# Performance work log

Hardware: AMD Instinct MI355X
Metric: run time of the kernel (lower is better)

## Reference

```python
import jax, jax.numpy as jnp
import numpy as np

N_EXPERTS = 8
D_MODEL = 1024
D_FF = 4096


def setup_inputs() -> dict:
    key = jax.random.key(0)
    k_x, k_idx, k_g, k_u, k_d = jax.random.split(key, 5)
    scale_in = 1.0 / np.sqrt(D_MODEL)
    scale_ff = 1.0 / np.sqrt(D_FF)
    return {
        "x": jax.random.normal(k_x, (2, 1024, D_MODEL), dtype=jnp.float32),
        "expert_idx": jax.random.randint(k_idx, (2, 1024), 0, N_EXPERTS, dtype=jnp.int64),
        "w_gate": jax.random.normal(k_g, (N_EXPERTS, D_MODEL, D_FF), dtype=jnp.float32) * scale_in,
        "w_up": jax.random.normal(k_u, (N_EXPERTS, D_MODEL, D_FF), dtype=jnp.float32) * scale_in,
        "w_down": jax.random.normal(k_d, (N_EXPERTS, D_FF, D_MODEL), dtype=jnp.float32) * scale_ff,
    }


def reference(x, expert_idx, w_gate, w_up, w_down):
    # x: [B, S, D]; expert_idx: [B, S] in [0, N_EXPERTS)
    B, S, D = x.shape
    x_flat = x.reshape(-1, D)                  # [T, D]
    idx_flat = expert_idx.reshape(-1)          # [T]
    out = jnp.zeros_like(x_flat)
    # Faithful per-expert dispatch: each token is processed by exactly one
    # expert's SwiGLU FFN; masked scatter-back combines results.
    for e in range(N_EXPERTS):
        mask = (idx_flat == e)[:, None]        # [T, 1]
        gate = jax.nn.silu(x_flat @ w_gate[e]) # [T, F]
        up = x_flat @ w_up[e]                  # [T, F]
        y = (gate * up) @ w_down[e]            # [T, D]
        out = jnp.where(mask, y, out)
    return out.reshape(B, S, D)
```

## Files before the change

kernel.cpp:

```cpp
#include <hip/hip_runtime.h>
#include <hip/hip_bf16.h>
#include <stdint.h>

#define N_EXPERTS 8
#define D_MODEL   1024
#define D_FF      4096
#define T_TOKENS  2048
#define MT1       128
#define MAXT1     24
#define MT2       64
#define MAXT2     40
#define BK        64
#define KP        72

typedef __attribute__((ext_vector_type(8))) short bf16x8;
typedef __attribute__((ext_vector_type(4))) float f32x4;

__device__ __forceinline__ short f2bf(float f) {
    union { float f; uint32_t u; } v; v.f = f;
    uint32_t u = v.u;
    return (short)((u + 0x7fffu + ((u >> 16) & 1u)) >> 16);
}

__device__ __forceinline__ uint32_t pack2bf(float a, float b) {
    __hip_bfloat162 h = __float22bfloat162_rn(make_float2(a, b));
    return *(uint32_t*)&h;
}

template<int STRIDE>
__device__ __forceinline__ void ldw16(float v[16], const float* __restrict__ src) {
#pragma unroll
    for (int j = 0; j < 16; ++j) v[j] = src[(size_t)j * STRIDE];
}

__device__ __forceinline__ void stw16(short* dst, const float v[16]) {
    uint4 w0, w1;
    w0.x = pack2bf(v[0], v[1]);  w0.y = pack2bf(v[2], v[3]);
    w0.z = pack2bf(v[4], v[5]);  w0.w = pack2bf(v[6], v[7]);
    w1.x = pack2bf(v[8], v[9]);  w1.y = pack2bf(v[10], v[11]);
    w1.z = pack2bf(v[12], v[13]); w1.w = pack2bf(v[14], v[15]);
    *(uint4*)dst = w0;
    *(uint4*)(dst + 8) = w1;
}


__global__ void moe_route(const int* __restrict__ idx, int* __restrict__ offsets,
                          int* __restrict__ nt1p, int* __restrict__ t1_e,
                          int* __restrict__ t1_p0, int* __restrict__ t1_end,
                          int* __restrict__ nt2p, int* __restrict__ t2_e,
                          int* __restrict__ t2_p0, int* __restrict__ t2_end) {
    __shared__ int cnt[N_EXPERTS];
    int tid = threadIdx.x;
    if (tid < N_EXPERTS) cnt[tid] = 0;
    __syncthreads();
    for (int t = tid; t < T_TOKENS; t += 256) atomicAdd(&cnt[idx[t]], 1);
    __syncthreads();
    if (tid == 0) {
        int off = 0, nt1 = 0, nt2 = 0;
        for (int e = 0; e < N_EXPERTS; ++e) {
            offsets[e] = off;
            int c = cnt[e], end = off + c;
            for (int i = 0; i < c; i += MT1) { t1_e[nt1] = e; t1_p0[nt1] = off + i; t1_end[nt1] = end; ++nt1; }
            for (int i = 0; i < c; i += MT2) { t2_e[nt2] = e; t2_p0[nt2] = off + i; t2_end[nt2] = end; ++nt2; }
            off = end;
        }
        offsets[N_EXPERTS] = off;
        *nt1p = nt1;
        *nt2p = nt2;
    }
}

__global__ void moe_gather(const float* __restrict__ x, const int* __restrict__ idx,
                           const int* __restrict__ offsets, int* __restrict__ cursor,
                           int* __restrict__ tok_of_row, short* __restrict__ Xg) {
    __shared__ int sp;
    int t = blockIdx.x;
    if (threadIdx.x == 0) {
        int e = idx[t];
        int p = offsets[e] + atomicAdd(&cursor[e], 1);
        tok_of_row[p] = t;
        sp = p;
    }
    __syncthreads();
    int p = sp;
    const float4* src = (const float4*)(x + (size_t)t * D_MODEL);
    uint2* dst = (uint2*)(Xg + (size_t)p * D_MODEL);
    int i = threadIdx.x;
    float4 v = src[i];
    uint2 o;
    o.x = pack2bf(v.x, v.y);
    o.y = pack2bf(v.z, v.w);
    dst[i] = o;
}


__launch_bounds__(256)
__global__ void moe_gemm1(const float* __restrict__ wg, const float* __restrict__ wu,
                          const short* __restrict__ Xg, short* __restrict__ h,
                          const int* __restrict__ tile_e, const int* __restrict__ tile_p0,
                          const int* __restrict__ tile_end, const int* __restrict__ ntiles) {
    int ti = blockIdx.y;
    if (ti >= *ntiles) return;
    int e = tile_e[ti], p0 = tile_p0[ti], pend = tile_end[ti];
    int n0 = blockIdx.x * 64;

    __shared__ short Bg[2][64][KP];
    __shared__ short Bu[2][64][KP];

    int tid = threadIdx.x;
    int nl = tid & 63, kc = tid >> 6;
    int lane = tid & 63, w = tid >> 6;
    int col = lane & 15, quad = lane >> 4;

    const float* wgb = wg + (size_t)e * D_MODEL * D_FF + (size_t)(kc * 16) * D_FF + n0 + nl;
    const float* wub = wu + (size_t)e * D_MODEL * D_FF + (size_t)(kc * 16) * D_FF + n0 + nl;

    int row0 = p0 + w * 32 + col;      if (row0 > T_TOKENS - 1) row0 = T_TOKENS - 1;
    int row1 = row0 + 16;              if (row1 > T_TOKENS - 1) row1 = T_TOKENS - 1;
    const short* a0p = Xg + (size_t)row0 * D_MODEL + quad * 8;
    const short* a1p = Xg + (size_t)row1 * D_MODEL + quad * 8;

    f32x4 accg[2][4], accu[2][4];
#pragma unroll
    for (int m = 0; m < 2; ++m)
#pragma unroll
        for (int nf = 0; nf < 4; ++nf) {
            accg[m][nf] = (f32x4){0,0,0,0};
            accu[m][nf] = (f32x4){0,0,0,0};
        }

    {
        float g0[16], u0[16];
        ldw16<D_FF>(g0, wgb);
        ldw16<D_FF>(u0, wub);
        stw16(&Bg[0][nl][kc * 16], g0);
        stw16(&Bu[0][nl][kc * 16], u0);
    }
    __syncthreads();

    bf16x8 a00 = *(const bf16x8*)(a0p);
    bf16x8 a01 = *(const bf16x8*)(a0p + 32);
    bf16x8 a10 = *(const bf16x8*)(a1p);
    bf16x8 a11 = *(const bf16x8*)(a1p + 32);

    const int NIT = D_MODEL / BK;
    int p = 0;
#pragma unroll 1
    for (int it = 0; it < NIT; ++it) {
        int kn = (it + 1 == NIT) ? 0 : (it + 1) * BK;
        float gn[16], un[16];
        ldw16<D_FF>(gn, wgb + (size_t)kn * D_FF);
        ldw16<D_FF>(un, wub + (size_t)kn * D_FF);
        bf16x8 a00n = *(const bf16x8*)(a0p + kn);
        bf16x8 a01n = *(const bf16x8*)(a0p + kn + 32);
        bf16x8 a10n = *(const bf16x8*)(a1p + kn);
        bf16x8 a11n = *(const bf16x8*)(a1p + kn + 32);

#pragma unroll
        for (int nf = 0; nf < 4; ++nf) {
            bf16x8 bg0 = *(const bf16x8*)&Bg[p][nf * 16 + col][quad * 8];
            bf16x8 bg1 = *(const bf16x8*)&Bg[p][nf * 16 + col][32 + quad * 8];
            bf16x8 bu0 = *(const bf16x8*)&Bu[p][nf * 16 + col][quad * 8];
            bf16x8 bu1 = *(const bf16x8*)&Bu[p][nf * 16 + col][32 + quad * 8];
            accg[0][nf] = __builtin_amdgcn_mfma_f32_16x16x32_bf16(a00, bg0, accg[0][nf], 0, 0, 0);
            accg[0][nf] = __builtin_amdgcn_mfma_f32_16x16x32_bf16(a01, bg1, accg[0][nf], 0, 0, 0);
            accg[1][nf] = __builtin_amdgcn_mfma_f32_16x16x32_bf16(a10, bg0, accg[1][nf], 0, 0, 0);
            accg[1][nf] = __builtin_amdgcn_mfma_f32_16x16x32_bf16(a11, bg1, accg[1][nf], 0, 0, 0);
            accu[0][nf] = __builtin_amdgcn_mfma_f32_16x16x32_bf16(a00, bu0, accu[0][nf], 0, 0, 0);
            accu[0][nf] = __builtin_amdgcn_mfma_f32_16x16x32_bf16(a01, bu1, accu[0][nf], 0, 0, 0);
            accu[1][nf] = __builtin_amdgcn_mfma_f32_16x16x32_bf16(a10, bu0, accu[1][nf], 0, 0, 0);
            accu[1][nf] = __builtin_amdgcn_mfma_f32_16x16x32_bf16(a11, bu1, accu[1][nf], 0, 0, 0);
        }

        stw16(&Bg[p ^ 1][nl][kc * 16], gn);
        stw16(&Bu[p ^ 1][nl][kc * 16], un);
        a00 = a00n; a01 = a01n; a10 = a10n; a11 = a11n;
        __syncthreads();
        p ^= 1;
    }

#pragma unroll
    for (int m = 0; m < 2; ++m) {
#pragma unroll
        for (int r = 0; r < 4; ++r) {
            int mr = p0 + w * 32 + m * 16 + quad * 4 + r;
            if (mr < pend) {
#pragma unroll
                for (int nf = 0; nf < 4; ++nf) {
                    float gv = accg[m][nf][r], uv = accu[m][nf][r];
                    float hv = (gv / (1.f + __expf(-gv))) * uv;
                    h[(size_t)mr * D_FF + n0 + nf * 16 + col] = f2bf(hv);
                }
            }
        }
    }
}


__launch_bounds__(256)
__global__ void moe_gemm2(const float* __restrict__ wd, const short* __restrict__ h,
                          const int* __restrict__ tok_of_row, float* __restrict__ out,
                          const int* __restrict__ tile_e, const int* __restrict__ tile_p0,
                          const int* __restrict__ tile_end, const int* __restrict__ ntiles) {
    int ti = blockIdx.y;
    if (ti >= *ntiles) return;
    int e = tile_e[ti], p0 = tile_p0[ti], pend = tile_end[ti];
    int d0 = blockIdx.x * 64;

    __shared__ short Bd[2][64][KP];

    int tid = threadIdx.x;
    int nl = tid & 63, kc = tid >> 6;
    int lane = tid & 63, w = tid >> 6;
    int col = lane & 15, quad = lane >> 4;

    const float* wb = wd + (size_t)e * D_FF * D_MODEL + (size_t)(kc * 16) * D_MODEL + d0 + nl;

    int row0 = p0 + w * 16 + col;      if (row0 > T_TOKENS - 1) row0 = T_TOKENS - 1;
    const short* a0p = h + (size_t)row0 * D_FF + quad * 8;

    f32x4 acc[4];
#pragma unroll
    for (int nf = 0; nf < 4; ++nf) acc[nf] = (f32x4){0,0,0,0};

    {
        float w0[16];
        ldw16<D_MODEL>(w0, wb);
        stw16(&Bd[0][nl][kc * 16], w0);
    }
    __syncthreads();

    bf16x8 a0 = *(const bf16x8*)(a0p);
    bf16x8 a1 = *(const bf16x8*)(a0p + 32);

    const int NIT = D_FF / BK;
    int p = 0;
#pragma unroll 1
    for (int it = 0; it < NIT; ++it) {
        int kn = (it + 1 == NIT) ? 0 : (it + 1) * BK;
        float wn[16];
        ldw16<D_MODEL>(wn, wb + (size_t)kn * D_MODEL);
        bf16x8 a0n = *(const bf16x8*)(a0p + kn);
        bf16x8 a1n = *(const bf16x8*)(a0p + kn + 32);

#pragma unroll
        for (int nf = 0; nf < 4; ++nf) {
            bf16x8 b0 = *(const bf16x8*)&Bd[p][nf * 16 + col][quad * 8];
            bf16x8 b1 = *(const bf16x8*)&Bd[p][nf * 16 + col][32 + quad * 8];
            acc[nf] = __builtin_amdgcn_mfma_f32_16x16x32_bf16(a0, b0, acc[nf], 0, 0, 0);
            acc[nf] = __builtin_amdgcn_mfma_f32_16x16x32_bf16(a1, b1, acc[nf], 0, 0, 0);
        }

        stw16(&Bd[p ^ 1][nl][kc * 16], wn);
        a0 = a0n; a1 = a1n;
        __syncthreads();
        p ^= 1;
    }

#pragma unroll
    for (int r = 0; r < 4; ++r) {
        int mr = p0 + w * 16 + quad * 4 + r;
        if (mr < pend) {
            int t = tok_of_row[mr];
#pragma unroll
            for (int nf = 0; nf < 4; ++nf)
                out[(size_t)t * D_MODEL + d0 + nf * 16 + col] = acc[nf][r];
        }
    }
}


extern "C" void kernel_launch(void* const* d_in, const int* in_sizes, int n_in,
                              void* d_out, int out_size, void* d_ws, size_t ws_size,
                              hipStream_t stream) {
    (void)in_sizes; (void)n_in; (void)out_size; (void)ws_size;
    const float* x   = (const float*)d_in[0];
    const int*   idx = (const int*)d_in[1];
    const float* wg  = (const float*)d_in[2];
    const float* wu  = (const float*)d_in[3];
    const float* wd  = (const float*)d_in[4];
    float* out = (float*)d_out;

    int* ws_i       = (int*)d_ws;
    int* cursor     = ws_i;
    int* offsets    = ws_i + 8;
    int* nt1        = ws_i + 20;
    int* nt2        = ws_i + 21;
    int* t1_e       = ws_i + 32;
    int* t1_p0      = ws_i + 56;
    int* t1_end     = ws_i + 80;
    int* t2_e       = ws_i + 104;
    int* t2_p0      = ws_i + 144;
    int* t2_end     = ws_i + 184;
    int* tok_of_row = ws_i + 256;

    short* Xg = (short*)((char*)d_ws + 16384);
    short* h  = (short*)((char*)d_ws + 16384 + (size_t)T_TOKENS * D_MODEL * 2);

    hipMemsetAsync(d_ws, 0, 128, stream);
    moe_route<<<dim3(1), 256, 0, stream>>>(idx, offsets, nt1, t1_e, t1_p0, t1_end,
                                           nt2, t2_e, t2_p0, t2_end);
    moe_gather<<<dim3(T_TOKENS), 256, 0, stream>>>(x, idx, offsets, cursor, tok_of_row, Xg);
    moe_gemm1<<<dim3(D_FF / 64, MAXT1), 256, 0, stream>>>(wg, wu, Xg, h,
                                                          t1_e, t1_p0, t1_end, nt1);
    moe_gemm2<<<dim3(D_MODEL / 64, MAXT2), 256, 0, stream>>>(wd, h, tok_of_row, out,
                                                             t2_e, t2_p0, t2_end, nt2);
}
```

Before: 508.0 us.

## Enlarge token tiles to 256 rows and split-K the down projection with atomics

Both GEMMs now use 256-token tiles, with each wave covering 64 rows, so every fp32 weight tile loaded and converted into LDS is reused across more tokens. This cuts repeated weight reads, which dominate traffic, especially in the down projection that previously used 64-row tiles. To keep enough blocks in flight, the down projection splits K into 8 slices that accumulate into a zero-initialised output via float atomicAdd. The trade-offs are higher register pressure, an extra memset, atomic contention, and slightly nondeterministic summation order.

```diff
diff --git a/kernel.cpp b/kernel.cpp
--- a/kernel.cpp
+++ b/kernel.cpp
@@ -6,10 +6,9 @@
 #define D_MODEL   1024
 #define D_FF      4096
 #define T_TOKENS  2048
-#define MT1       128
-#define MAXT1     24
-#define MT2       64
-#define MAXT2     40
+#define MT        256
+#define MAXT      16
+#define KSPLIT    8
 #define BK        64
 #define KP        72
 
@@ -45,10 +44,8 @@
 
 
 __global__ void moe_route(const int* __restrict__ idx, int* __restrict__ offsets,
-                          int* __restrict__ nt1p, int* __restrict__ t1_e,
-                          int* __restrict__ t1_p0, int* __restrict__ t1_end,
-                          int* __restrict__ nt2p, int* __restrict__ t2_e,
-                          int* __restrict__ t2_p0, int* __restrict__ t2_end) {
+                          int* __restrict__ ntp, int* __restrict__ t_e,
+                          int* __restrict__ t_p0, int* __restrict__ t_end) {
     __shared__ int cnt[N_EXPERTS];
     int tid = threadIdx.x;
     if (tid < N_EXPERTS) cnt[tid] = 0;
@@ -56,17 +53,15 @@
     for (int t = tid; t < T_TOKENS; t += 256) atomicAdd(&cnt[idx[t]], 1);
     __syncthreads();
     if (tid == 0) {
-        int off = 0, nt1 = 0, nt2 = 0;
+        int off = 0, nt = 0;
         for (int e = 0; e < N_EXPERTS; ++e) {
             offsets[e] = off;
             int c = cnt[e], end = off + c;
-            for (int i = 0; i < c; i += MT1) { t1_e[nt1] = e; t1_p0[nt1] = off + i; t1_end[nt1] = end; ++nt1; }
-            for (int i = 0; i < c; i += MT2) { t2_e[nt2] = e; t2_p0[nt2] = off + i; t2_end[nt2] = end; ++nt2; }
+            for (int i = 0; i < c; i += MT) { t_e[nt] = e; t_p0[nt] = off + i; t_end[nt] = end; ++nt; }
             off = end;
         }
         offsets[N_EXPERTS] = off;
-        *nt1p = nt1;
-        *nt2p = nt2;
+        *ntp = nt;
     }
 }
 
@@ -94,14 +89,14 @@
 }
 
 
-__launch_bounds__(256)
+__launch_bounds__(256, 2)
 __global__ void moe_gemm1(const float* __restrict__ wg, const float* __restrict__ wu,
                           const short* __restrict__ Xg, short* __restrict__ h,
-                          const int* __restrict__ tile_e, const int* __restrict__ tile_p0,
-                          const int* __restrict__ tile_end, const int* __restrict__ ntiles) {
+                          const int* __restrict__ t_e, const int* __restrict__ t_p0,
+                          const int* __restrict__ t_end, const int* __restrict__ ntp) {
     int ti = blockIdx.y;
-    if (ti >= *ntiles) return;
-    int e = tile_e[ti], p0 = tile_p0[ti], pend = tile_end[ti];
+    if (ti >= *ntp) return;
+    int e = t_e[ti], p0 = t_p0[ti], pend = t_end[ti];
     int n0 = blockIdx.x * 64;
 
     __shared__ short Bg[2][64][KP];
@@ -115,14 +110,17 @@
     const float* wgb = wg + (size_t)e * D_MODEL * D_FF + (size_t)(kc * 16) * D_FF + n0 + nl;
     const float* wub = wu + (size_t)e * D_MODEL * D_FF + (size_t)(kc * 16) * D_FF + n0 + nl;
 
-    int row0 = p0 + w * 32 + col;      if (row0 > T_TOKENS - 1) row0 = T_TOKENS - 1;
-    int row1 = row0 + 16;              if (row1 > T_TOKENS - 1) row1 = T_TOKENS - 1;
-    const short* a0p = Xg + (size_t)row0 * D_MODEL + quad * 8;
-    const short* a1p = Xg + (size_t)row1 * D_MODEL + quad * 8;
-
-    f32x4 accg[2][4], accu[2][4];
-#pragma unroll
-    for (int m = 0; m < 2; ++m)
+    const short* ap[4];
+#pragma unroll
+    for (int m = 0; m < 4; ++m) {
+        int r = p0 + w * 64 + m * 16 + col;
+        if (r > T_TOKENS - 1) r = T_TOKENS - 1;
+        ap[m] = Xg + (size_t)r * D_MODEL + quad * 8;
+    }
+
+    f32x4 accg[4][4], accu[4][4];
+#pragma unroll
+    for (int m = 0; m < 4; ++m)
 #pragma unroll
         for (int nf = 0; nf < 4; ++nf) {
             accg[m][nf] = (f32x4){0,0,0,0};
@@ -137,11 +135,6 @@
         stw16(&Bu[0][nl][kc * 16], u0);
     }
     __syncthreads();
-
-    bf16x8 a00 = *(const bf16x8*)(a0p);
-    bf16x8 a01 = *(const bf16x8*)(a0p + 32);
-    bf16x8 a10 = *(const bf16x8*)(a1p);
-    bf16x8 a11 = *(const bf16x8*)(a1p + 32);
 
     const int NIT = D_MODEL / BK;
     int p = 0;
@@ -151,39 +144,40 @@
         float gn[16], un[16];
         ldw16<D_FF>(gn, wgb + (size_t)kn * D_FF);
         ldw16<D_FF>(un, wub + (size_t)kn * D_FF);
-        bf16x8 a00n = *(const bf16x8*)(a0p + kn);
-        bf16x8 a01n = *(const bf16x8*)(a0p + kn + 32);
-        bf16x8 a10n = *(const bf16x8*)(a1p + kn);
-        bf16x8 a11n = *(const bf16x8*)(a1p + kn + 32);
-
-#pragma unroll
-        for (int nf = 0; nf < 4; ++nf) {
-            bf16x8 bg0 = *(const bf16x8*)&Bg[p][nf * 16 + col][quad * 8];
-            bf16x8 bg1 = *(const bf16x8*)&Bg[p][nf * 16 + col][32 + quad * 8];
-            bf16x8 bu0 = *(const bf16x8*)&Bu[p][nf * 16 + col][quad * 8];
-            bf16x8 bu1 = *(const bf16x8*)&Bu[p][nf * 16 + col][32 + quad * 8];
-            accg[0][nf] = __builtin_amdgcn_mfma_f32_16x16x32_bf16(a00, bg0, accg[0][nf], 0, 0, 0);
-            accg[0][nf] = __builtin_amdgcn_mfma_f32_16x16x32_bf16(a01, bg1, accg[0][nf], 0, 0, 0);
-            accg[1][nf] = __builtin_amdgcn_mfma_f32_16x16x32_bf16(a10, bg0, accg[1][nf], 0, 0, 0);
-            accg[1][nf] = __builtin_amdgcn_mfma_f32_16x16x32_bf16(a11, bg1, accg[1][nf], 0, 0, 0);
-            accu[0][nf] = __builtin_amdgcn_mfma_f32_16x16x32_bf16(a00, bu0, accu[0][nf], 0, 0, 0);
-            accu[0][nf] = __builtin_amdgcn_mfma_f32_16x16x32_bf16(a01, bu1, accu[0][nf], 0, 0, 0);
-            accu[1][nf] = __builtin_amdgcn_mfma_f32_16x16x32_bf16(a10, bu0, accu[1][nf], 0, 0, 0);
-            accu[1][nf] = __builtin_amdgcn_mfma_f32_16x16x32_bf16(a11, bu1, accu[1][nf], 0, 0, 0);
+        int kb = it * BK;
+
+#pragma unroll
+        for (int ks = 0; ks < 2; ++ks) {
+            bf16x8 a0 = *(const bf16x8*)(ap[0] + kb + ks * 32);
+            bf16x8 a1 = *(const bf16x8*)(ap[1] + kb + ks * 32);
+            bf16x8 a2 = *(const bf16x8*)(ap[2] + kb + ks * 32);
+            bf16x8 a3 = *(const bf16x8*)(ap[3] + kb + ks * 32);
+#pragma unroll
+            for (int nf = 0; nf < 4; ++nf) {
+                bf16x8 bg = *(const bf16x8*)&Bg[p][nf * 16 + col][ks * 32 + quad * 8];
+                bf16x8 bu = *(const bf16x8*)&Bu[p][nf * 16 + col][ks * 32 + quad * 8];
+                accg[0][nf] = __builtin_amdgcn_mfma_f32_16x16x32_bf16(a0, bg, accg[0][nf], 0, 0, 0);
+                accg[1][nf] = __builtin_amdgcn_mfma_f32_16x16x32_bf16(a1, bg, accg[1][nf], 0, 0, 0);
+                accg[2][nf] = __builtin_amdgcn_mfma_f32_16x16x32_bf16(a2, bg, accg[2][nf], 0, 0, 0);
+                accg[3][nf] = __builtin_amdgcn_mfma_f32_16x16x32_bf16(a3, bg, accg[3][nf], 0, 0, 0);
+                accu[0][nf] = __builtin_amdgcn_mfma_f32_16x16x32_bf16(a0, bu, accu[0][nf], 0, 0, 0);
+                accu[1][nf] = __builtin_amdgcn_mfma_f32_16x16x32_bf16(a1, bu, accu[1][nf], 0, 0, 0);
+                accu[2][nf] = __builtin_amdgcn_mfma_f32_16x16x32_bf16(a2, bu, accu[2][nf], 0, 0, 0);
+                accu[3][nf] = __builtin_amdgcn_mfma_f32_16x16x32_bf16(a3, bu, accu[3][nf], 0, 0, 0);
+            }
         }
 
         stw16(&Bg[p ^ 1][nl][kc * 16], gn);
         stw16(&Bu[p ^ 1][nl][kc * 16], un);
-        a00 = a00n; a01 = a01n; a10 = a10n; a11 = a11n;
         __syncthreads();
         p ^= 1;
     }
 
 #pragma unroll
-    for (int m = 0; m < 2; ++m) {
+    for (int m = 0; m < 4; ++m) {
 #pragma unroll
         for (int r = 0; r < 4; ++r) {
-            int mr = p0 + w * 32 + m * 16 + quad * 4 + r;
+            int mr = p0 + w * 64 + m * 16 + quad * 4 + r;
             if (mr < pend) {
 #pragma unroll
                 for (int nf = 0; nf < 4; ++nf) {
@@ -197,15 +191,16 @@
 }
 
 
-__launch_bounds__(256)
+__launch_bounds__(256, 3)
 __global__ void moe_gemm2(const float* __restrict__ wd, const short* __restrict__ h,
                           const int* __restrict__ tok_of_row, float* __restrict__ out,
-                          const int* __restrict__ tile_e, const int* __restrict__ tile_p0,
-                          const int* __restrict__ tile_end, const int* __restrict__ ntiles) {
+                          const int* __restrict__ t_e, const int* __restrict__ t_p0,
+                          const int* __restrict__ t_end, const int* __restrict__ ntp) {
     int ti = blockIdx.y;
-    if (ti >= *ntiles) return;
-    int e = tile_e[ti], p0 = tile_p0[ti], pend = tile_end[ti];
+    if (ti >= *ntp) return;
+    int e = t_e[ti], p0 = t_p0[ti], pend = t_end[ti];
     int d0 = blockIdx.x * 64;
+    int Koff = blockIdx.z * (D_FF / KSPLIT);
 
     __shared__ short Bd[2][64][KP];
 
@@ -214,14 +209,21 @@
     int lane = tid & 63, w = tid >> 6;
     int col = lane & 15, quad = lane >> 4;
 
-    const float* wb = wd + (size_t)e * D_FF * D_MODEL + (size_t)(kc * 16) * D_MODEL + d0 + nl;
-
-    int row0 = p0 + w * 16 + col;      if (row0 > T_TOKENS - 1) row0 = T_TOKENS - 1;
-    const short* a0p = h + (size_t)row0 * D_FF + quad * 8;
-
-    f32x4 acc[4];
-#pragma unroll
-    for (int nf = 0; nf < 4; ++nf) acc[nf] = (f32x4){0,0,0,0};
+    const float* wb = wd + (size_t)e * D_FF * D_MODEL + (size_t)(Koff + kc * 16) * D_MODEL + d0 + nl;
+
+    const short* ap[4];
+#pragma unroll
+    for (int m = 0; m < 4; ++m) {
+        int r = p0 + w * 64 + m * 16 + col;
+        if (r > T_TOKENS - 1) r = T_TOKENS - 1;
+        ap[m] = h + (size_t)r * D_FF + Koff + quad * 8;
+    }
+
+    f32x4 acc[4][4];
+#pragma unroll
+    for (int m = 0; m < 4; ++m)
+#pragma unroll
+        for (int nf = 0; nf < 4; ++nf) acc[m][nf] = (f32x4){0,0,0,0};
 
     {
         float w0[16];
@@ -230,41 +232,47 @@
     }
     __syncthreads();
 
-    bf16x8 a0 = *(const bf16x8*)(a0p);
-    bf16x8 a1 = *(const bf16x8*)(a0p + 32);
-
-    const int NIT = D_FF / BK;
+    const int NIT = (D_FF / KSPLIT) / BK;
     int p = 0;
 #pragma unroll 1
     for (int it = 0; it < NIT; ++it) {
         int kn = (it + 1 == NIT) ? 0 : (it + 1) * BK;
         float wn[16];
         ldw16<D_MODEL>(wn, wb + (size_t)kn * D_MODEL);
-        bf16x8 a0n = *(const bf16x8*)(a0p + kn);
-        bf16x8 a1n = *(const bf16x8*)(a0p + kn + 32);
-
-#pragma unroll
-        for (int nf = 0; nf < 4; ++nf) {
-            bf16x8 b0 = *(const bf16x8*)&Bd[p][nf * 16 + col][quad * 8];
-            bf16x8 b1 = *(const bf16x8*)&Bd[p][nf * 16 + col][32 + quad * 8];
-            acc[nf] = __builtin_amdgcn_mfma_f32_16x16x32_bf16(a0, b0, acc[nf], 0, 0, 0);
-            acc[nf] = __builtin_amdgcn_mfma_f32_16x16x32_bf16(a1, b1, acc[nf], 0, 0, 0);
+        int kb = it * BK;
+
+#pragma unroll
+        for (int ks = 0; ks < 2; ++ks) {
+            bf16x8 a0 = *(const bf16x8*)(ap[0] + kb + ks * 32);
+            bf16x8 a1 = *(const bf16x8*)(ap[1] + kb + ks * 32);
+            bf16x8 a2 = *(const bf16x8*)(ap[2] + kb + ks * 32);
+            bf16x8 a3 = *(const bf16x8*)(ap[3] + kb + ks * 32);
+#pragma unroll
+            for (int nf = 0; nf < 4; ++nf) {
+                bf16x8 b = *(const bf16x8*)&Bd[p][nf * 16 + col][ks * 32 + quad * 8];
+                acc[0][nf] = __builtin_amdgcn_mfma_f32_16x16x32_bf16(a0, b, acc[0][nf], 0, 0, 0);
+                acc[1][nf] = __builtin_amdgcn_mfma_f32_16x16x32_bf16(a1, b, acc[1][nf], 0, 0, 0);
+                acc[2][nf] = __builtin_amdgcn_mfma_f32_16x16x32_bf16(a2, b, acc[2][nf], 0, 0, 0);
+                acc[3][nf] = __builtin_amdgcn_mfma_f32_16x16x32_bf16(a3, b, acc[3][nf], 0, 0, 0);
+            }
         }
 
         stw16(&Bd[p ^ 1][nl][kc * 16], wn);
-        a0 = a0n; a1 = a1n;
         __syncthreads();
         p ^= 1;
     }
 
 #pragma unroll
-    for (int r = 0; r < 4; ++r) {
-        int mr = p0 + w * 16 + quad * 4 + r;
-        if (mr < pend) {
-            int t = tok_of_row[mr];
-#pragma unroll
-            for (int nf = 0; nf < 4; ++nf)
-                out[(size_t)t * D_MODEL + d0 + nf * 16 + col] = acc[nf][r];
+    for (int m = 0; m < 4; ++m) {
+#pragma unroll
+        for (int r = 0; r < 4; ++r) {
+            int mr = p0 + w * 64 + m * 16 + quad * 4 + r;
+            if (mr < pend) {
+                int t = tok_of_row[mr];
+#pragma unroll
+                for (int nf = 0; nf < 4; ++nf)
+                    atomicAdd(&out[(size_t)t * D_MODEL + d0 + nf * 16 + col], acc[m][nf][r]);
+            }
         }
     }
 }
@@ -284,25 +292,21 @@
     int* ws_i       = (int*)d_ws;
     int* cursor     = ws_i;
     int* offsets    = ws_i + 8;
-    int* nt1        = ws_i + 20;
-    int* nt2        = ws_i + 21;
-    int* t1_e       = ws_i + 32;
-    int* t1_p0      = ws_i + 56;
-    int* t1_end     = ws_i + 80;
-    int* t2_e       = ws_i + 104;
-    int* t2_p0      = ws_i + 144;
-    int* t2_end     = ws_i + 184;
+    int* nt         = ws_i + 20;
+    int* t_e        = ws_i + 32;
+    int* t_p0       = ws_i + 48;
+    int* t_end      = ws_i + 64;
     int* tok_of_row = ws_i + 256;
 
     short* Xg = (short*)((char*)d_ws + 16384);
     short* h  = (short*)((char*)d_ws + 16384 + (size_t)T_TOKENS * D_MODEL * 2);
 
     hipMemsetAsync(d_ws, 0, 128, stream);
-    moe_route<<<dim3(1), 256, 0, stream>>>(idx, offsets, nt1, t1_e, t1_p0, t1_end,
-                                           nt2, t2_e, t2_p0, t2_end);
+    hipMemsetAsync(out, 0, (size_t)T_TOKENS * D_MODEL * sizeof(float), stream);
+    moe_route<<<dim3(1), 256, 0, stream>>>(idx, offsets, nt, t_e, t_p0, t_end);
     moe_gather<<<dim3(T_TOKENS), 256, 0, stream>>>(x, idx, offsets, cursor, tok_of_row, Xg);
-    moe_gemm1<<<dim3(D_FF / 64, MAXT1), 256, 0, stream>>>(wg, wu, Xg, h,
-                                                          t1_e, t1_p0, t1_end, nt1);
-    moe_gemm2<<<dim3(D_MODEL / 64, MAXT2), 256, 0, stream>>>(wd, h, tok_of_row, out,
-                                                             t2_e, t2_p0, t2_end, nt2);
-}
+    moe_gemm1<<<dim3(D_FF / 64, MAXT), 256, 0, stream>>>(wg, wu, Xg, h,
+                                                         t_e, t_p0, t_end, nt);
+    moe_gemm2<<<dim3(D_MODEL / 64, MAXT, KSPLIT), 256, 0, stream>>>(wd, h, tok_of_row, out,
+                                                                    t_e, t_p0, t_end, nt);
+}
```

After: 559.6 us. +10.2%, slower.

## Split gemm1 gate/up across 512-thread blocks and split-K gemm2 with atomics

Applied to the files above, without the earlier changes.

gemm1 now launches 512 threads per block, with half the waves computing the gate projection and half the up projection. The SiLU gate values are exchanged through shared memory, which halves per-wave accumulator registers and doubles the waves per block. gemm2 splits the D_FF reduction four ways over a grid z dimension and accumulates into a zeroed output with float atomicAdd. This raises parallelism for the small-N down projection, at the cost of an output memset, atomic traffic and non-deterministic summation order.

```diff
diff --git a/kernel.cpp b/kernel.cpp
--- a/kernel.cpp
+++ b/kernel.cpp
@@ -10,6 +10,7 @@
 #define MAXT1     24
 #define MT2       64
 #define MAXT2     40
+#define KSPLIT    4
 #define BK        64
 #define KP        72
 
@@ -94,7 +95,7 @@
 }
 
 
-__launch_bounds__(256)
+__launch_bounds__(512)
 __global__ void moe_gemm1(const float* __restrict__ wg, const float* __restrict__ wu,
                           const short* __restrict__ Xg, short* __restrict__ h,
                           const int* __restrict__ tile_e, const int* __restrict__ tile_p0,
@@ -104,37 +105,35 @@
     int e = tile_e[ti], p0 = tile_p0[ti], pend = tile_end[ti];
     int n0 = blockIdx.x * 64;
 
-    __shared__ short Bg[2][64][KP];
-    __shared__ short Bu[2][64][KP];
+    __shared__ short Bsh[2][2][64][KP];
 
     int tid = threadIdx.x;
-    int nl = tid & 63, kc = tid >> 6;
+    int st = tid & 255, matS = tid >> 8;
+    int nl = st & 63, kc = st >> 6;
     int lane = tid & 63, w = tid >> 6;
+    int mat = w >> 2, wm = w & 3;
     int col = lane & 15, quad = lane >> 4;
 
-    const float* wgb = wg + (size_t)e * D_MODEL * D_FF + (size_t)(kc * 16) * D_FF + n0 + nl;
-    const float* wub = wu + (size_t)e * D_MODEL * D_FF + (size_t)(kc * 16) * D_FF + n0 + nl;
-
-    int row0 = p0 + w * 32 + col;      if (row0 > T_TOKENS - 1) row0 = T_TOKENS - 1;
+    const float* wsrc = (matS ? wu : wg) + (size_t)e * D_MODEL * D_FF
+                        + (size_t)(kc * 16) * D_FF + n0 + nl;
+    short* std0 = &Bsh[matS][0][nl][kc * 16];
+    short* std1 = &Bsh[matS][1][nl][kc * 16];
+
+    int row0 = p0 + wm * 32 + col;     if (row0 > T_TOKENS - 1) row0 = T_TOKENS - 1;
     int row1 = row0 + 16;              if (row1 > T_TOKENS - 1) row1 = T_TOKENS - 1;
     const short* a0p = Xg + (size_t)row0 * D_MODEL + quad * 8;
     const short* a1p = Xg + (size_t)row1 * D_MODEL + quad * 8;
 
-    f32x4 accg[2][4], accu[2][4];
+    f32x4 acc[2][4];
 #pragma unroll
     for (int m = 0; m < 2; ++m)
 #pragma unroll
-        for (int nf = 0; nf < 4; ++nf) {
-            accg[m][nf] = (f32x4){0,0,0,0};
-            accu[m][nf] = (f32x4){0,0,0,0};
-        }
+        for (int nf = 0; nf < 4; ++nf) acc[m][nf] = (f32x4){0,0,0,0};
 
     {
-        float g0[16], u0[16];
-        ldw16<D_FF>(g0, wgb);
-        ldw16<D_FF>(u0, wub);
-        stw16(&Bg[0][nl][kc * 16], g0);
-        stw16(&Bu[0][nl][kc * 16], u0);
+        float g0[16];
+        ldw16<D_FF>(g0, wsrc);
+        stw16(std0, g0);
     }
     __syncthreads();
 
@@ -142,15 +141,16 @@
     bf16x8 a01 = *(const bf16x8*)(a0p + 32);
     bf16x8 a10 = *(const bf16x8*)(a1p);
     bf16x8 a11 = *(const bf16x8*)(a1p + 32);
+
+    auto Bp = Bsh[mat];
 
     const int NIT = D_MODEL / BK;
     int p = 0;
 #pragma unroll 1
     for (int it = 0; it < NIT; ++it) {
         int kn = (it + 1 == NIT) ? 0 : (it + 1) * BK;
-        float gn[16], un[16];
-        ldw16<D_FF>(gn, wgb + (size_t)kn * D_FF);
-        ldw16<D_FF>(un, wub + (size_t)kn * D_FF);
+        float gn[16];
+        ldw16<D_FF>(gn, wsrc + (size_t)kn * D_FF);
         bf16x8 a00n = *(const bf16x8*)(a0p + kn);
         bf16x8 a01n = *(const bf16x8*)(a0p + kn + 32);
         bf16x8 a10n = *(const bf16x8*)(a1p + kn);
@@ -158,41 +158,50 @@
 
 #pragma unroll
         for (int nf = 0; nf < 4; ++nf) {
-            bf16x8 bg0 = *(const bf16x8*)&Bg[p][nf * 16 + col][quad * 8];
-            bf16x8 bg1 = *(const bf16x8*)&Bg[p][nf * 16 + col][32 + quad * 8];
-            bf16x8 bu0 = *(const bf16x8*)&Bu[p][nf * 16 + col][quad * 8];
-            bf16x8 bu1 = *(const bf16x8*)&Bu[p][nf * 16 + col][32 + quad * 8];
-            accg[0][nf] = __builtin_amdgcn_mfma_f32_16x16x32_bf16(a00, bg0, accg[0][nf], 0, 0, 0);
-            accg[0][nf] = __builtin_amdgcn_mfma_f32_16x16x32_bf16(a01, bg1, accg[0][nf], 0, 0, 0);
-            accg[1][nf] = __builtin_amdgcn_mfma_f32_16x16x32_bf16(a10, bg0, accg[1][nf], 0, 0, 0);
-            accg[1][nf] = __builtin_amdgcn_mfma_f32_16x16x32_bf16(a11, bg1, accg[1][nf], 0, 0, 0);
-            accu[0][nf] = __builtin_amdgcn_mfma_f32_16x16x32_bf16(a00, bu0, accu[0][nf], 0, 0, 0);
-            accu[0][nf] = __builtin_amdgcn_mfma_f32_16x16x32_bf16(a01, bu1, accu[0][nf], 0, 0, 0);
-            accu[1][nf] = __builtin_amdgcn_mfma_f32_16x16x32_bf16(a10, bu0, accu[1][nf], 0, 0, 0);
-            accu[1][nf] = __builtin_amdgcn_mfma_f32_16x16x32_bf16(a11, bu1, accu[1][nf], 0, 0, 0);
+            bf16x8 b0 = *(const bf16x8*)&Bp[p][nf * 16 + col][quad * 8];
+            bf16x8 b1 = *(const bf16x8*)&Bp[p][nf * 16 + col][32 + quad * 8];
+            acc[0][nf] = __builtin_amdgcn_mfma_f32_16x16x32_bf16(a00, b0, acc[0][nf], 0, 0, 0);
+            acc[0][nf] = __builtin_amdgcn_mfma_f32_16x16x32_bf16(a01, b1, acc[0][nf], 0, 0, 0);
+            acc[1][nf] = __builtin_amdgcn_mfma_f32_16x16x32_bf16(a10, b0, acc[1][nf], 0, 0, 0);
+            acc[1][nf] = __builtin_amdgcn_mfma_f32_16x16x32_bf16(a11, b1, acc[1][nf], 0, 0, 0);
         }
 
-        stw16(&Bg[p ^ 1][nl][kc * 16], gn);
-        stw16(&Bu[p ^ 1][nl][kc * 16], un);
+        stw16(p ? std0 : std1, gn);
         a00 = a00n; a01 = a01n; a10 = a10n; a11 = a11n;
         __syncthreads();
         p ^= 1;
     }
 
-#pragma unroll
-    for (int m = 0; m < 2; ++m) {
-#pragma unroll
-        for (int r = 0; r < 4; ++r) {
-            int mr = p0 + w * 32 + m * 16 + quad * 4 + r;
-            if (mr < pend) {
+    float* ExF = (float*)&Bsh[0][0][0][0];
+    if (mat == 0) {
+#pragma unroll
+        for (int m = 0; m < 2; ++m)
+#pragma unroll
+            for (int r = 0; r < 4; ++r) {
+                int rl = wm * 32 + m * 16 + quad * 4 + r;
 #pragma unroll
                 for (int nf = 0; nf < 4; ++nf) {
-                    float gv = accg[m][nf][r], uv = accu[m][nf][r];
-                    float hv = (gv / (1.f + __expf(-gv))) * uv;
-                    h[(size_t)mr * D_FF + n0 + nf * 16 + col] = f2bf(hv);
+                    float gv = acc[m][nf][r];
+                    ExF[rl * 65 + nf * 16 + col] = gv / (1.f + __expf(-gv));
                 }
             }
-        }
+    }
+    __syncthreads();
+    if (mat == 1) {
+#pragma unroll
+        for (int m = 0; m < 2; ++m)
+#pragma unroll
+            for (int r = 0; r < 4; ++r) {
+                int rl = wm * 32 + m * 16 + quad * 4 + r;
+                int mr = p0 + rl;
+                if (mr < pend) {
+#pragma unroll
+                    for (int nf = 0; nf < 4; ++nf) {
+                        float hv = ExF[rl * 65 + nf * 16 + col] * acc[m][nf][r];
+                        h[(size_t)mr * D_FF + n0 + nf * 16 + col] = f2bf(hv);
+                    }
+                }
+            }
     }
 }
 
@@ -206,6 +215,7 @@
     if (ti >= *ntiles) return;
     int e = tile_e[ti], p0 = tile_p0[ti], pend = tile_end[ti];
     int d0 = blockIdx.x * 64;
+    int Koff = blockIdx.z * (D_FF / KSPLIT);
 
     __shared__ short Bd[2][64][KP];
 
@@ -214,10 +224,10 @@
     int lane = tid & 63, w = tid >> 6;
     int col = lane & 15, quad = lane >> 4;
 
-    const float* wb = wd + (size_t)e * D_FF * D_MODEL + (size_t)(kc * 16) * D_MODEL + d0 + nl;
+    const float* wb = wd + (size_t)e * D_FF * D_MODEL + (size_t)(Koff + kc * 16) * D_MODEL + d0 + nl;
 
     int row0 = p0 + w * 16 + col;      if (row0 > T_TOKENS - 1) row0 = T_TOKENS - 1;
-    const short* a0p = h + (size_t)row0 * D_FF + quad * 8;
+    const short* a0p = h + (size_t)row0 * D_FF + Koff + quad * 8;
 
     f32x4 acc[4];
 #pragma unroll
@@ -233,7 +243,7 @@
     bf16x8 a0 = *(const bf16x8*)(a0p);
     bf16x8 a1 = *(const bf16x8*)(a0p + 32);
 
-    const int NIT = D_FF / BK;
+    const int NIT = (D_FF / KSPLIT) / BK;
     int p = 0;
 #pragma unroll 1
     for (int it = 0; it < NIT; ++it) {
@@ -264,7 +274,7 @@
             int t = tok_of_row[mr];
 #pragma unroll
             for (int nf = 0; nf < 4; ++nf)
-                out[(size_t)t * D_MODEL + d0 + nf * 16 + col] = acc[nf][r];
+                atomicAdd(&out[(size_t)t * D_MODEL + d0 + nf * 16 + col], acc[nf][r]);
         }
     }
 }
@@ -298,11 +308,12 @@
     short* h  = (short*)((char*)d_ws + 16384 + (size_t)T_TOKENS * D_MODEL * 2);
 
     hipMemsetAsync(d_ws, 0, 128, stream);
+    hipMemsetAsync(out, 0, (size_t)T_TOKENS * D_MODEL * sizeof(float), stream);
     moe_route<<<dim3(1), 256, 0, stream>>>(idx, offsets, nt1, t1_e, t1_p0, t1_end,
                                            nt2, t2_e, t2_p0, t2_end);
     moe_gather<<<dim3(T_TOKENS), 256, 0, stream>>>(x, idx, offsets, cursor, tok_of_row, Xg);
-    moe_gemm1<<<dim3(D_FF / 64, MAXT1), 256, 0, stream>>>(wg, wu, Xg, h,
+    moe_gemm1<<<dim3(D_FF / 64, MAXT1), 512, 0, stream>>>(wg, wu, Xg, h,
                                                           t1_e, t1_p0, t1_end, nt1);
-    moe_gemm2<<<dim3(D_MODEL / 64, MAXT2), 256, 0, stream>>>(wd, h, tok_of_row, out,
-                                                             t2_e, t2_p0, t2_end, nt2);
-}
+    moe_gemm2<<<dim3(D_MODEL / 64, MAXT2, KSPLIT), 256, 0, stream>>>(wd, h, tok_of_row, out,
+                                                                     t2_e, t2_p0, t2_end, nt2);
+}
```

Measured after the change: 554.0 us. 1.09x slower.
